# Performance work log

Measured on AMD Instinct MI355X. Metric: run time of the kernel, lower is better.

## Reference

```python
import jax, jax.numpy as jnp
import numpy as np

B, N, D, F, H, C, L = 64, 8192, 5, 16, 4, 4, 4
NEG_SLOPE = 0.2


def setup_inputs() -> dict:
    key = jax.random.key(0)
    ks = jax.random.split(key, 16)
    lin = lambda k, fi, fo: (jax.random.normal(k, (fi, fo), jnp.float32) / np.sqrt(fi)).astype(jnp.float32)
    x = jax.random.normal(ks[0], (B, N, F), jnp.float32)
    agent_nodes = jax.random.randint(ks[1], (B,), 0, N, dtype=jnp.int32)
    neighbors = jax.random.randint(ks[2], (N, D), 0, N, dtype=jnp.int32)
    # GATv2 params (L layers, all 16 -> 4 heads x 4 = 16)
    Wl = jax.random.normal(ks[3], (L, F, H, C), jnp.float32) / np.sqrt(F)
    Wr = jax.random.normal(ks[4], (L, F, H, C), jnp.float32) / np.sqrt(F)
    att_w = jax.random.normal(ks[5], (L, H, C), jnp.float32) / np.sqrt(C)
    bias = jnp.zeros((L, H * C), jnp.float32)
    # global classifier 16->32->64, edge classifier 99->16->8->1
    Wg1, bg1 = lin(ks[6], H * C, 2 * H * C), jnp.zeros(2 * H * C, jnp.float32)
    Wg2, bg2 = lin(ks[7], 2 * H * C, 4 * H * C), jnp.zeros(4 * H * C, jnp.float32)
    e_in = 2 * H * C + 3 + 4 * H * C  # 99
    We1, be1 = lin(ks[8], e_in, H * C), jnp.zeros(H * C, jnp.float32)
    We2, be2 = lin(ks[9], H * C, H * C // 2), jnp.zeros(H * C // 2, jnp.float32)
    We3, be3 = lin(ks[10], H * C // 2, 1), jnp.zeros(1, jnp.float32)
    return dict(x=x, agent_nodes=agent_nodes, neighbors=neighbors, Wl=Wl, Wr=Wr,
                att_w=att_w, bias=bias, Wg1=Wg1, bg1=bg1, Wg2=Wg2, bg2=bg2,
                We1=We1, be1=be1, We2=We2, be2=be2, We3=We3, be3=be3)


def _gatv2_layer(h, src, dst, wl, wr, a, b, n_nodes):
    # h: [B,N,Fin]; wl/wr: [Fin,H,C]; a: [H,C]; b: [H*C]
    xl = jnp.einsum('bnf,fhc->bnhc', h, wl)   # source transform
    xr = jnp.einsum('bnf,fhc->bnhc', h, wr)   # target transform
    hs = xl[:, src]                            # [B,E,H,C]
    ht = xr[:, dst]
    logit = jnp.einsum('behc,hc->beh', jax.nn.leaky_relu(hs + ht, NEG_SLOPE), a)
    lt = logit.transpose(1, 0, 2)              # [E,B,H] (segment ops need E first)
    m = jax.ops.segment_max(lt, dst, num_segments=n_nodes)
    w = jnp.exp(lt - m[dst])
    s = jax.ops.segment_sum(w, dst, num_segments=n_nodes)
    alpha = w / (s[dst] + 1e-16)               # [E,B,H] softmax over in-edges of dst
    msg = alpha[..., None] * hs.transpose(1, 0, 2, 3)
    out = jax.ops.segment_sum(msg, dst, num_segments=n_nodes)  # [N,B,H,C]
    return out.transpose(1, 0, 2, 3).reshape(h.shape[0], n_nodes, -1) + b


def reference(x, agent_nodes, neighbors, Wl, Wr, att_w, bias,
              Wg1, bg1, Wg2, bg2, We1, be1, We2, be2, We3, be3):
    Bn, Nn, _ = x.shape
    Dd = neighbors.shape[1]
    loop = jnp.arange(Nn, dtype=neighbors.dtype)
    src = jnp.concatenate([jnp.repeat(loop, Dd), loop])   # add_self_loops
    dst = jnp.concatenate([neighbors.reshape(-1), loop])
    h = x
    for i in range(Wl.shape[0]):
        h = _gatv2_layer(h, src, dst, Wl[i], Wr[i], att_w[i], bias[i], Nn)
    # global mean aggregation -> 2 SlimFC(tanh)
    agg = jnp.tanh(h.mean(axis=1) @ Wg1 + bg1)
    agg = jnp.tanh(agg @ Wg2 + bg2)                        # [B,64]
    # agent out-edges: source node + its D neighbors
    nb = neighbors[agent_nodes]                            # [B,D]
    bi = jnp.arange(Bn)
    source = h[bi, agent_nodes]                            # [B,16]
    target = h[bi[:, None], nb]                            # [B,D,16]
    tok = jnp.eye(3, dtype=h.dtype)                        # 3 one-hot act tokens
    feats = jnp.concatenate([
        jnp.broadcast_to(source[:, None, None, :], (Bn, 3, Dd, source.shape[-1])),
        jnp.broadcast_to(tok[None, :, None, :], (Bn, 3, Dd, 3)),
        jnp.broadcast_to(target[:, None, :, :], (Bn, 3, Dd, target.shape[-1])),
        jnp.broadcast_to(agg[:, None, None, :], (Bn, 3, Dd, agg.shape[-1])),
    ], axis=-1)                                            # [B,3,D,99]
    e = jnp.tanh(feats @ We1 + be1)
    e = jnp.tanh(e @ We2 + be2)
    e = (e @ We3 + be3)[..., 0]                            # [B,3,D]
    # logits[b, turn*D + move] (convert_multidiscrete_action_to_discrete)
    return e.reshape(Bn, 3 * Dd)
```

## Files before the change

### kernel.cpp

```cpp
#include <hip/hip_runtime.h>
#include <hip/hip_fp16.h>
#include <cmath>

#define NNODES 8192
#define NB 64
#define ND 5
#define MAXDEG 64
#define NBLK_L 2048



__global__ void k_fill0(int* __restrict__ cnt, int* __restrict__ slot) {
  int v = blockIdx.x*blockDim.x + threadIdx.x;
  cnt[v] = 1;
  slot[v*MAXDEG] = v;
}

__global__ void k_fill(const int* __restrict__ nbr, int* __restrict__ cnt, int* __restrict__ slot) {
  int i = blockIdx.x*blockDim.x + threadIdx.x;
  int v = nbr[i];
  int pos = atomicAdd(&cnt[v], 1);
  slot[v*MAXDEG + pos] = i/ND;
}


__global__ void __launch_bounds__(256)
k_t0(const float* __restrict__ x, const float* __restrict__ Wl0, const float* __restrict__ Wr0,
     __half* __restrict__ xl0, __half* __restrict__ xr0) {
  int gid = blockIdx.x*blockDim.x + threadIdx.x;
  int n = gid >> 6;
  int b = gid & 63;
  const float4* src = (const float4*)(x + (((size_t)b*NNODES + n) << 4));
  float hv[16];
  #pragma unroll
  for (int q = 0; q < 4; ++q) *(float4*)(hv+4*q) = src[q];
  float yl[16], yr[16];
  #pragma unroll
  for (int j = 0; j < 16; ++j) { yl[j] = 0.f; yr[j] = 0.f; }
  #pragma unroll
  for (int f = 0; f < 16; ++f) {
    float hf = hv[f];
    #pragma unroll
    for (int j = 0; j < 16; ++j) {
      yl[j] = fmaf(hf, Wl0[f*16+j], yl[j]);
      yr[j] = fmaf(hf, Wr0[f*16+j], yr[j]);
    }
  }
  size_t idx = ((size_t)n << 10) + (b << 4);
  __half2 lh[8], rh[8];
  #pragma unroll
  for (int j = 0; j < 8; ++j) {
    lh[j] = __floats2half2_rn(yl[2*j], yl[2*j+1]);
    rh[j] = __floats2half2_rn(yr[2*j], yr[2*j+1]);
  }
  float4* ld = (float4*)(xl0 + idx);
  ld[0] = *(float4*)&lh[0]; ld[1] = *(float4*)&lh[4];
  float4* rd = (float4*)(xr0 + idx);
  rd[0] = *(float4*)&rh[0]; rd[1] = *(float4*)&rh[4];
}


template<bool LAST>
__global__ void __launch_bounds__(256)
k_layer(const __half* __restrict__ xlin, const __half* __restrict__ xrin,
        __half* __restrict__ xlout, __half* __restrict__ xrout,
        const float* __restrict__ WlNext, const float* __restrict__ WrNext,
        const float* __restrict__ att, const float* __restrict__ bias,
        const int* __restrict__ cnt, const int* __restrict__ slot,
        float* __restrict__ h, float* __restrict__ meanpart) {
  __shared__ float msm[4096];
  int gid = blockIdx.x*blockDim.x + threadIdx.x;
  int v = gid >> 6;
  int b = gid & 63;
  int w = threadIdx.x >> 6;
  size_t boff = (size_t)(b << 4);

  float xr[16];
  {
    const float4* rp = (const float4*)(xrin + ((size_t)v << 10) + boff);
    float4 r0 = rp[0], r1 = rp[1];
    const __half2* pa = (const __half2*)&r0;
    const __half2* pb = (const __half2*)&r1;
    #pragma unroll
    for (int q = 0; q < 4; ++q) { float2 f = __half22float2(pa[q]); xr[2*q] = f.x; xr[2*q+1] = f.y; }
    #pragma unroll
    for (int q = 0; q < 4; ++q) { float2 f = __half22float2(pb[q]); xr[8+2*q] = f.x; xr[8+2*q+1] = f.y; }
  }
  float aw[16];
  #pragma unroll
  for (int j = 0; j < 16; ++j) aw[j] = att[j];

  float s4[4] = {0.f, 0.f, 0.f, 0.f};
  float acc[16];
  #pragma unroll
  for (int j = 0; j < 16; ++j) acc[j] = 0.f;

  int deg = cnt[v];
  const int* sl = slot + v*MAXDEG;

  auto loadrow = [&](int u, float4& r0, float4& r1) {
    const float4* sp = (const float4*)(xlin + ((size_t)u << 10) + boff);
    r0 = sp[0]; r1 = sp[1];
  };
  auto process = [&](const float4& r0, const float4& r1) {
    float t[16];
    const __half2* pa = (const __half2*)&r0;
    const __half2* pb = (const __half2*)&r1;
    #pragma unroll
    for (int q = 0; q < 4; ++q) { float2 f = __half22float2(pa[q]); t[2*q] = f.x; t[2*q+1] = f.y; }
    #pragma unroll
    for (int q = 0; q < 4; ++q) { float2 f = __half22float2(pb[q]); t[8+2*q] = f.x; t[8+2*q+1] = f.y; }
    #pragma unroll
    for (int hh = 0; hh < 4; ++hh) {
      float lg = 0.f;
      #pragma unroll
      for (int c = 0; c < 4; ++c) {
        float z = t[hh*4+c] + xr[hh*4+c];
        z = (z >= 0.f) ? z : 0.2f*z;
        lg = fmaf(z, aw[hh*4+c], lg);
      }
      float p = __expf(lg);
      s4[hh] += p;
      #pragma unroll
      for (int c = 0; c < 4; ++c) acc[hh*4+c] = fmaf(p, t[hh*4+c], acc[hh*4+c]);
    }
  };

  float4 a0, a1, b0, b1, c0, c1;
  loadrow(sl[0], a0, a1);
  if (deg > 1) loadrow(sl[1], b0, b1);
  if (deg > 2) loadrow(sl[2], c0, c1);
  int e = 0;
  for (; e+3 <= deg; e += 3) {
    process(a0, a1); if (e+3 < deg) loadrow(sl[e+3], a0, a1);
    process(b0, b1); if (e+4 < deg) loadrow(sl[e+4], b0, b1);
    process(c0, c1); if (e+5 < deg) loadrow(sl[e+5], c0, c1);
  }
  if (e < deg)   process(a0, a1);
  if (e+1 < deg) process(b0, b1);

  float o[16];
  #pragma unroll
  for (int hh = 0; hh < 4; ++hh) {
    float inv = 1.f / s4[hh];
    #pragma unroll
    for (int c = 0; c < 4; ++c) o[hh*4+c] = fmaf(acc[hh*4+c], inv, bias[hh*4+c]);
  }

  if (!LAST) {
    float yl[16], yr[16];
    #pragma unroll
    for (int j = 0; j < 16; ++j) { yl[j] = 0.f; yr[j] = 0.f; }
    #pragma unroll
    for (int f = 0; f < 16; ++f) {
      float of = o[f];
      #pragma unroll
      for (int j = 0; j < 16; ++j) {
        yl[j] = fmaf(of, WlNext[f*16+j], yl[j]);
        yr[j] = fmaf(of, WrNext[f*16+j], yr[j]);
      }
    }
    __half2 lh[8], rh[8];
    #pragma unroll
    for (int j = 0; j < 8; ++j) {
      lh[j] = __floats2half2_rn(yl[2*j], yl[2*j+1]);
      rh[j] = __floats2half2_rn(yr[2*j], yr[2*j+1]);
    }
    size_t idx = ((size_t)v << 10) + boff;
    float4* ld = (float4*)(xlout + idx);
    ld[0] = *(float4*)&lh[0]; ld[1] = *(float4*)&lh[4];
    float4* rd = (float4*)(xrout + idx);
    rd[0] = *(float4*)&rh[0]; rd[1] = *(float4*)&rh[4];
  } else {
    float4* hd = (float4*)(h + ((size_t)v << 10) + boff);
    #pragma unroll
    for (int q = 0; q < 4; ++q) hd[q] = *(float4*)(o+4*q);
    #pragma unroll
    for (int j = 0; j < 16; ++j) msm[(w << 10) + (b << 4) + j] = o[j];
    __syncthreads();
    for (int i = threadIdx.x; i < 1024; i += 256) {
      float s = msm[i] + msm[1024+i] + msm[2048+i] + msm[3072+i];
      meanpart[(size_t)blockIdx.x*1024 + i] = s;
    }
  }
}


__global__ void __launch_bounds__(256)
k_tail(const float* __restrict__ h, const int* __restrict__ agent,
       const int* __restrict__ nbr, const float* __restrict__ meanpart,
       const float* __restrict__ Wg1, const float* __restrict__ bg1,
       const float* __restrict__ Wg2, const float* __restrict__ bg2,
       const float* __restrict__ We1, const float* __restrict__ be1,
       const float* __restrict__ We2, const float* __restrict__ be2,
       const float* __restrict__ We3, const float* __restrict__ be3,
       float* __restrict__ out) {
  int b = blockIdx.x;
  int t = threadIdx.x;
  __shared__ float red[256];
  __shared__ float mean[16], g1[32], aggs[64];
  __shared__ float srcv[16];
  __shared__ float tgt[5][16];
  __shared__ float e1s[15][16];
  __shared__ float e2s[15][8];
  int an = agent[b];

  {
    int hc = t & 15, grp = t >> 4;
    float s = 0.f;
    for (int p = grp*128; p < grp*128+128; ++p) s += meanpart[(size_t)p*1024 + b*16 + hc];
    red[t] = s;
    __syncthreads();
    if (t < 16) {
      float m = 0.f;
      for (int g = 0; g < 16; ++g) m += red[g*16 + t];
      mean[t] = m * (1.0f/NNODES);
    }
  }
  if (t >= 64 && t < 80) srcv[t-64] = h[((size_t)an << 10) + (b << 4) + (t-64)];
  if (t >= 96 && t < 176) {
    int d = (t-96)/16, k = (t-96)%16;
    int nn = nbr[an*ND + d];
    tgt[d][k] = h[((size_t)nn << 10) + (b << 4) + k];
  }
  __syncthreads();
  if (t < 32) {
    float a = bg1[t];
    for (int f = 0; f < 16; ++f) a = fmaf(mean[f], Wg1[f*32+t], a);
    g1[t] = tanhf(a);
  }
  __syncthreads();
  if (t < 64) {
    float a = bg2[t];
    for (int f = 0; f < 32; ++f) a = fmaf(g1[f], Wg2[f*64+t], a);
    aggs[t] = tanhf(a);
  }
  __syncthreads();
  if (t < 240) {
    int j = t & 15, td = t >> 4;
    int tk = td/5, d = td%5;
    float a = be1[j];
    for (int k = 0; k < 16; ++k) a = fmaf(srcv[k],  We1[k*16+j],      a);
    a += We1[(16+tk)*16 + j];
    for (int k = 0; k < 16; ++k) a = fmaf(tgt[d][k], We1[(19+k)*16+j], a);
    for (int k = 0; k < 64; ++k) a = fmaf(aggs[k],  We1[(35+k)*16+j], a);
    e1s[td][j] = tanhf(a);
  }
  __syncthreads();
  if (t < 120) {
    int j = t & 7, td = t >> 3;
    float a = be2[j];
    for (int k = 0; k < 16; ++k) a = fmaf(e1s[td][k], We2[k*8+j], a);
    e2s[td][j] = tanhf(a);
  }
  __syncthreads();
  if (t < 15) {
    float a = be3[0];
    for (int k = 0; k < 8; ++k) a = fmaf(e2s[t][k], We3[k], a);
    out[b*15 + t] = a;
  }
}


extern "C" void kernel_launch(void* const* d_in, const int* in_sizes, int n_in,
                              void* d_out, int out_size, void* d_ws, size_t ws_size,
                              hipStream_t stream) {
  const float* x     = (const float*)d_in[0];
  const int*   agent = (const int*)  d_in[1];
  const int*   nbr   = (const int*)  d_in[2];
  const float* Wl    = (const float*)d_in[3];
  const float* Wr    = (const float*)d_in[4];
  const float* att   = (const float*)d_in[5];
  const float* bias  = (const float*)d_in[6];
  const float* Wg1   = (const float*)d_in[7];
  const float* bg1   = (const float*)d_in[8];
  const float* Wg2   = (const float*)d_in[9];
  const float* bg2   = (const float*)d_in[10];
  const float* We1   = (const float*)d_in[11];
  const float* be1   = (const float*)d_in[12];
  const float* We2   = (const float*)d_in[13];
  const float* be2   = (const float*)d_in[14];
  const float* We3   = (const float*)d_in[15];
  const float* be3   = (const float*)d_in[16];
  float* out = (float*)d_out;

  char* ws = (char*)d_ws;
  size_t off = 0;
  auto alloc = [&](size_t bytes) -> void* {
    void* p = ws + off;
    off += (bytes + 255) & ~(size_t)255;
    return p;
  };
  const size_t HBYTES  = (size_t)NNODES*NB*16*sizeof(float);
  const size_t XBYTES  = (size_t)NNODES*NB*16*sizeof(__half);
  float*  h    = (float*)alloc(HBYTES);
  __half* xlA  = (__half*)alloc(XBYTES);
  __half* xlB  = (__half*)alloc(XBYTES);
  __half* xrA  = (__half*)alloc(XBYTES);
  __half* xrB  = (__half*)alloc(XBYTES);
  int* cnt     = (int*)alloc(NNODES*sizeof(int));
  int* slot    = (int*)alloc((size_t)NNODES*MAXDEG*sizeof(int));
  float* meanpart = (float*)alloc((size_t)NBLK_L*1024*sizeof(float));

  k_fill0<<<NNODES/256, 256, 0, stream>>>(cnt, slot);
  k_fill<<<NNODES*ND/256, 256, 0, stream>>>(nbr, cnt, slot);

  k_t0<<<NBLK_L, 256, 0, stream>>>(x, Wl, Wr, xlA, xrA);

  k_layer<false><<<NBLK_L, 256, 0, stream>>>(xlA, xrA, xlB, xrB, Wl + 256, Wr + 256,
                                             att,      bias,      cnt, slot, nullptr, nullptr);
  k_layer<false><<<NBLK_L, 256, 0, stream>>>(xlB, xrB, xlA, xrA, Wl + 512, Wr + 512,
                                             att + 16, bias + 16, cnt, slot, nullptr, nullptr);
  k_layer<false><<<NBLK_L, 256, 0, stream>>>(xlA, xrA, xlB, xrB, Wl + 768, Wr + 768,
                                             att + 32, bias + 32, cnt, slot, nullptr, nullptr);
  k_layer<true ><<<NBLK_L, 256, 0, stream>>>(xlB, xrB, nullptr, nullptr, nullptr, nullptr,
                                             att + 48, bias + 48, cnt, slot, h, meanpart);

  k_tail<<<NB, 256, 0, stream>>>(h, agent, nbr, meanpart,
                                 Wg1, bg1, Wg2, bg2,
                                 We1, be1, We2, be2, We3, be3, out);
}
```

Measured before the change: 254.1 us.

## Fuse graph build into first transform, skip unneeded final writes, deepen gather prefetch

Merges the two adjacency-building kernels into a single-block init kernel plus extra blocks appended to the first transform kernel, which saves launches. Adds a 'needed' mask so the last layer writes final node features only for agent nodes and their neighbors, and stores them as half precision. Replaces the 3-deep rotating edge prefetch with six upfront loads plus a one-ahead prefetch for the rest. In exchange it uses more registers, adds a serial single-block init, and the stored tail features lose some precision.

```diff
diff --git a/kernel.cpp b/kernel.cpp
--- a/kernel.cpp
+++ b/kernel.cpp
@@ -10,23 +10,38 @@
 
 
 
-__global__ void k_fill0(int* __restrict__ cnt, int* __restrict__ slot) {
-  int v = blockIdx.x*blockDim.x + threadIdx.x;
-  cnt[v] = 1;
-  slot[v*MAXDEG] = v;
-}
-
-__global__ void k_fill(const int* __restrict__ nbr, int* __restrict__ cnt, int* __restrict__ slot) {
-  int i = blockIdx.x*blockDim.x + threadIdx.x;
-  int v = nbr[i];
-  int pos = atomicAdd(&cnt[v], 1);
-  slot[v*MAXDEG + pos] = i/ND;
+__global__ void __launch_bounds__(1024)
+k_init(const int* __restrict__ agent, const int* __restrict__ nbr,
+       int* __restrict__ cnt, int* __restrict__ slot, int* __restrict__ needed) {
+  int t = threadIdx.x;
+  for (int v = t; v < NNODES; v += 1024) {
+    cnt[v] = 1;
+    slot[v*MAXDEG] = v;
+    needed[v] = 0;
+  }
+  __syncthreads();
+  if (t < NB) {
+    int an = agent[t];
+    needed[an] = 1;
+    #pragma unroll
+    for (int d = 0; d < ND; ++d) needed[nbr[an*ND + d]] = 1;
+  }
 }
 
 
 __global__ void __launch_bounds__(256)
-k_t0(const float* __restrict__ x, const float* __restrict__ Wl0, const float* __restrict__ Wr0,
-     __half* __restrict__ xl0, __half* __restrict__ xr0) {
+k_t0fill(const float* __restrict__ x, const float* __restrict__ Wl0, const float* __restrict__ Wr0,
+         __half* __restrict__ xl0, __half* __restrict__ xr0,
+         const int* __restrict__ nbr, int* __restrict__ cnt, int* __restrict__ slot) {
+  if (blockIdx.x >= NBLK_L) {
+    int i = (blockIdx.x - NBLK_L)*256 + threadIdx.x;
+    if (i < NNODES*ND) {
+      int v = nbr[i];
+      int pos = atomicAdd(&cnt[v], 1);
+      slot[v*MAXDEG + pos] = i/ND;
+    }
+    return;
+  }
   int gid = blockIdx.x*blockDim.x + threadIdx.x;
   int n = gid >> 6;
   int b = gid & 63;
@@ -67,7 +82,8 @@
         const float* __restrict__ WlNext, const float* __restrict__ WrNext,
         const float* __restrict__ att, const float* __restrict__ bias,
         const int* __restrict__ cnt, const int* __restrict__ slot,
-        float* __restrict__ h, float* __restrict__ meanpart) {
+        const int* __restrict__ needed, __half* __restrict__ h,
+        float* __restrict__ meanpart) {
   __shared__ float msm[4096];
   int gid = blockIdx.x*blockDim.x + threadIdx.x;
   int v = gid >> 6;
@@ -126,18 +142,25 @@
     }
   };
 
-  float4 a0, a1, b0, b1, c0, c1;
-  loadrow(sl[0], a0, a1);
-  if (deg > 1) loadrow(sl[1], b0, b1);
-  if (deg > 2) loadrow(sl[2], c0, c1);
-  int e = 0;
-  for (; e+3 <= deg; e += 3) {
-    process(a0, a1); if (e+3 < deg) loadrow(sl[e+3], a0, a1);
-    process(b0, b1); if (e+4 < deg) loadrow(sl[e+4], b0, b1);
-    process(c0, c1); if (e+5 < deg) loadrow(sl[e+5], c0, c1);
-  }
-  if (e < deg)   process(a0, a1);
-  if (e+1 < deg) process(b0, b1);
+  float4 r00,r01, r10,r11, r20,r21, r30,r31, r40,r41, r50,r51, p0,p1;
+  loadrow(sl[0], r00, r01);
+  if (deg > 1) loadrow(sl[1], r10, r11);
+  if (deg > 2) loadrow(sl[2], r20, r21);
+  if (deg > 3) loadrow(sl[3], r30, r31);
+  if (deg > 4) loadrow(sl[4], r40, r41);
+  if (deg > 5) loadrow(sl[5], r50, r51);
+  if (deg > 6) loadrow(sl[6], p0, p1);
+  process(r00, r01);
+  if (deg > 1) process(r10, r11);
+  if (deg > 2) process(r20, r21);
+  if (deg > 3) process(r30, r31);
+  if (deg > 4) process(r40, r41);
+  if (deg > 5) process(r50, r51);
+  for (int e = 6; e < deg; ++e) {
+    float4 c0 = p0, c1 = p1;
+    if (e+1 < deg) loadrow(sl[e+1], p0, p1);
+    process(c0, c1);
+  }
 
   float o[16];
   #pragma unroll
@@ -172,9 +195,13 @@
     float4* rd = (float4*)(xrout + idx);
     rd[0] = *(float4*)&rh[0]; rd[1] = *(float4*)&rh[4];
   } else {
-    float4* hd = (float4*)(h + ((size_t)v << 10) + boff);
-    #pragma unroll
-    for (int q = 0; q < 4; ++q) hd[q] = *(float4*)(o+4*q);
+    if (needed[v]) {
+      __half2 oh[8];
+      #pragma unroll
+      for (int j = 0; j < 8; ++j) oh[j] = __floats2half2_rn(o[2*j], o[2*j+1]);
+      float4* hd = (float4*)(h + ((size_t)v << 10) + boff);
+      hd[0] = *(float4*)&oh[0]; hd[1] = *(float4*)&oh[4];
+    }
     #pragma unroll
     for (int j = 0; j < 16; ++j) msm[(w << 10) + (b << 4) + j] = o[j];
     __syncthreads();
@@ -187,7 +214,7 @@
 
 
 __global__ void __launch_bounds__(256)
-k_tail(const float* __restrict__ h, const int* __restrict__ agent,
+k_tail(const __half* __restrict__ h, const int* __restrict__ agent,
        const int* __restrict__ nbr, const float* __restrict__ meanpart,
        const float* __restrict__ Wg1, const float* __restrict__ bg1,
        const float* __restrict__ Wg2, const float* __restrict__ bg2,
@@ -217,11 +244,11 @@
       mean[t] = m * (1.0f/NNODES);
     }
   }
-  if (t >= 64 && t < 80) srcv[t-64] = h[((size_t)an << 10) + (b << 4) + (t-64)];
+  if (t >= 64 && t < 80) srcv[t-64] = __half2float(h[((size_t)an << 10) + (b << 4) + (t-64)]);
   if (t >= 96 && t < 176) {
     int d = (t-96)/16, k = (t-96)%16;
     int nn = nbr[an*ND + d];
-    tgt[d][k] = h[((size_t)nn << 10) + (b << 4) + k];
+    tgt[d][k] = __half2float(h[((size_t)nn << 10) + (b << 4) + k]);
   }
   __syncthreads();
   if (t < 32) {
@@ -291,30 +318,28 @@
     off += (bytes + 255) & ~(size_t)255;
     return p;
   };
-  const size_t HBYTES  = (size_t)NNODES*NB*16*sizeof(float);
   const size_t XBYTES  = (size_t)NNODES*NB*16*sizeof(__half);
-  float*  h    = (float*)alloc(HBYTES);
+  __half* h    = (__half*)alloc(XBYTES);
   __half* xlA  = (__half*)alloc(XBYTES);
   __half* xlB  = (__half*)alloc(XBYTES);
   __half* xrA  = (__half*)alloc(XBYTES);
   __half* xrB  = (__half*)alloc(XBYTES);
   int* cnt     = (int*)alloc(NNODES*sizeof(int));
+  int* needed  = (int*)alloc(NNODES*sizeof(int));
   int* slot    = (int*)alloc((size_t)NNODES*MAXDEG*sizeof(int));
   float* meanpart = (float*)alloc((size_t)NBLK_L*1024*sizeof(float));
 
-  k_fill0<<<NNODES/256, 256, 0, stream>>>(cnt, slot);
-  k_fill<<<NNODES*ND/256, 256, 0, stream>>>(nbr, cnt, slot);
-
-  k_t0<<<NBLK_L, 256, 0, stream>>>(x, Wl, Wr, xlA, xrA);
+  k_init<<<1, 1024, 0, stream>>>(agent, nbr, cnt, slot, needed);
+  k_t0fill<<<NBLK_L + NNODES*ND/256, 256, 0, stream>>>(x, Wl, Wr, xlA, xrA, nbr, cnt, slot);
 
   k_layer<false><<<NBLK_L, 256, 0, stream>>>(xlA, xrA, xlB, xrB, Wl + 256, Wr + 256,
-                                             att,      bias,      cnt, slot, nullptr, nullptr);
+                                             att,      bias,      cnt, slot, needed, nullptr, nullptr);
   k_layer<false><<<NBLK_L, 256, 0, stream>>>(xlB, xrB, xlA, xrA, Wl + 512, Wr + 512,
-                                             att + 16, bias + 16, cnt, slot, nullptr, nullptr);
+                                             att + 16, bias + 16, cnt, slot, needed, nullptr, nullptr);
   k_layer<false><<<NBLK_L, 256, 0, stream>>>(xlA, xrA, xlB, xrB, Wl + 768, Wr + 768,
-                                             att + 32, bias + 32, cnt, slot, nullptr, nullptr);
+                                             att + 32, bias + 32, cnt, slot, needed, nullptr, nullptr);
   k_layer<true ><<<NBLK_L, 256, 0, stream>>>(xlB, xrB, nullptr, nullptr, nullptr, nullptr,
-                                             att + 48, bias + 48, cnt, slot, h, meanpart);
+                                             att + 48, bias + 48, cnt, slot, needed, h, meanpart);
 
   k_tail<<<NB, 256, 0, stream>>>(h, agent, nbr, meanpart,
                                  Wg1, bg1, Wg2, bg2,
```

New measurement: 245.9 us. 1.03x faster.
